# Kernel tuning notes

Measured on AMD Instinct MI355X. Metric: run time of the kernel, lower is better.

The kernel has to match this reference:

```python
import jax, jax.numpy as jnp
import numpy as np

MODEL_DIM = 1024
BATCH = 8
SEQ = 4096


def setup_inputs() -> dict:
    key = jax.random.key(0)
    x = jax.random.normal(key, (BATCH, SEQ, MODEL_DIM), dtype=jnp.float32)
    return {"input": x}


def _positional_encoding(seq_len: int, d_model: int, dtype) -> jnp.ndarray:
    # Faithful to the original: value = pos / 10000 ** (2*dim/d_model),
    # even dim -> sin(value), odd dim -> cos(value) (same raw-index frequency).
    pos = jnp.arange(seq_len, dtype=jnp.float32)[:, None]          # [S, 1]
    dim = jnp.arange(d_model, dtype=jnp.float32)[None, :]          # [1, D]
    inv_freq = jnp.power(jnp.float32(10000.0), -2.0 * dim / d_model)
    angle = pos * inv_freq                                          # [S, D]
    pe = jnp.where(jnp.arange(d_model)[None, :] % 2 == 0,
                   jnp.sin(angle), jnp.cos(angle))
    return pe.astype(dtype)


def reference(input) -> jnp.ndarray:
    B, S, D = input.shape
    pe = _positional_encoding(S, D, input.dtype)                    # [S, D]
    return input + pe[None, :, :]
```

## Files before the change

kernel.cpp:

```cpp
#include <hip/hip_runtime.h>
#include <stdint.h>


#define D_MODEL 1024
#define C_FREQ (-0.025952563241307517f)

__device__ float pe_val(int s, int d) {
    float angle = (float)s * exp2f(C_FREQ * (float)d);
    return (d & 1) ? cosf(angle) : sinf(angle);
}

__device__ uint32_t f2bf_rne(float f) {
    uint32_t b = __float_as_uint(f);
    return (b + 0x7FFFu + ((b >> 16) & 1u)) >> 16;
}

__global__ void detect_kernel(const uint16_t* in, int* flag) {
    __shared__ int bad;
    if (threadIdx.x == 0) bad = 0;
    __syncthreads();
    uint16_t u = in[threadIdx.x];
    int e = (u >> 7) & 0xFF;
    if (!(e == 0 || (e >= 96 && e <= 135))) bad = 1;
    __syncthreads();
    if (threadIdx.x == 0) *flag = (bad ? 0 : 1);
}

__global__ void pe_kernel(const void* vin, void* vout, const int* flag, int n) {
    __shared__ int bf16_s;
    if (threadIdx.x == 0) bf16_s = *flag;
    __syncthreads();
    const int is_bf16 = bf16_s;
    const int tid = blockIdx.x * blockDim.x + threadIdx.x;
    const int nth = gridDim.x * blockDim.x;

    if (is_bf16) {
        const uint32_t* in = (const uint32_t*)vin;
        uint32_t* out = (uint32_t*)vout;
        const int nw = n >> 1;
        for (int i = tid; i < nw; i += nth) {
            const int e0 = i << 1;
            const int d = e0 & (D_MODEL - 1);
            const int s = (e0 >> 10) & 4095;
            const float p0 = pe_val(s, d);
            const float p1 = pe_val(s, d + 1);
            const uint32_t w = in[i];
            const float x0 = __uint_as_float((w & 0xFFFFu) << 16);
            const float x1 = __uint_as_float(w & 0xFFFF0000u);
            out[i] = f2bf_rne(x0 + p0) | (f2bf_rne(x1 + p1) << 16);
        }
    } else {
        const float* in = (const float*)vin;
        float* out = (float*)vout;
        for (int i = tid; i < n; i += nth) {
            const int d = i & (D_MODEL - 1);
            const int s = (i >> 10) & 4095;
            out[i] = in[i] + pe_val(s, d);
        }
    }
}

extern "C" void kernel_launch(void* const* d_in, const int* in_sizes, int n_in,
                              void* d_out, int out_size, void* d_ws, size_t ws_size,
                              hipStream_t stream) {
    const void* x = d_in[0];
    int* flag = (int*)d_ws;
    detect_kernel<<<1, 256, 0, stream>>>((const uint16_t*)x, flag);
    pe_kernel<<<4096, 256, 0, stream>>>(x, d_out, flag, out_size);
}
```

Baseline: 235.9 us.

## Compute PE once per position and reuse across batch with vectorized nontemporal IO

Replaces the dtype-detecting grid-stride kernel with a single fp32 kernel in which each thread computes four PE values once and applies them to all eight batch rows. Loads and stores are 16-byte vectors with nontemporal hints, and the detect kernel launch is dropped. This removes redundant transcendental evaluation across the batch and the extra launch. In exchange it hardcodes the fp32 path and the fixed shapes.

After: 231.0 us. -2.1%, faster.

```diff
diff --git a/kernel.cpp b/kernel.cpp
--- a/kernel.cpp
+++ b/kernel.cpp
@@ -2,69 +2,47 @@
 #include <stdint.h>
 
 
-#define D_MODEL 1024
-#define C_FREQ (-0.025952563241307517f)
+constexpr int MODEL_DIM = 1024;
+constexpr int SEQ = 4096;
+constexpr int BATCH = 8;
+constexpr int SD = SEQ * MODEL_DIM;
+constexpr float C_FREQ = -0.025952563241307517f;
 
-__device__ float pe_val(int s, int d) {
-    float angle = (float)s * exp2f(C_FREQ * (float)d);
-    return (d & 1) ? cosf(angle) : sinf(angle);
-}
+typedef float v4f __attribute__((ext_vector_type(4)));
 
-__device__ uint32_t f2bf_rne(float f) {
-    uint32_t b = __float_as_uint(f);
-    return (b + 0x7FFFu + ((b >> 16) & 1u)) >> 16;
-}
+__global__ __launch_bounds__(256) void pe_add_kernel(
+    const float* __restrict__ xin, float* __restrict__ xout)
+{
+    const int t = blockIdx.x * blockDim.x + threadIdx.x;
+    const int s = t >> 8;
+    const int dbase = (t & 255) << 2;
 
-__global__ void detect_kernel(const uint16_t* in, int* flag) {
-    __shared__ int bad;
-    if (threadIdx.x == 0) bad = 0;
-    __syncthreads();
-    uint16_t u = in[threadIdx.x];
-    int e = (u >> 7) & 0xFF;
-    if (!(e == 0 || (e >= 96 && e <= 135))) bad = 1;
-    __syncthreads();
-    if (threadIdx.x == 0) *flag = (bad ? 0 : 1);
-}
+    const float pos = (float)s;
+    float pe[4];
+#pragma unroll
+    for (int j = 0; j < 4; ++j) {
+        const float angle = pos * exp2f(C_FREQ * (float)(dbase + j));
+        pe[j] = (j & 1) ? cosf(angle) : sinf(angle);
+    }
+    v4f pv;
+    pv.x = pe[0]; pv.y = pe[1]; pv.z = pe[2]; pv.w = pe[3];
 
-__global__ void pe_kernel(const void* vin, void* vout, const int* flag, int n) {
-    __shared__ int bf16_s;
-    if (threadIdx.x == 0) bf16_s = *flag;
-    __syncthreads();
-    const int is_bf16 = bf16_s;
-    const int tid = blockIdx.x * blockDim.x + threadIdx.x;
-    const int nth = gridDim.x * blockDim.x;
-
-    if (is_bf16) {
-        const uint32_t* in = (const uint32_t*)vin;
-        uint32_t* out = (uint32_t*)vout;
-        const int nw = n >> 1;
-        for (int i = tid; i < nw; i += nth) {
-            const int e0 = i << 1;
-            const int d = e0 & (D_MODEL - 1);
-            const int s = (e0 >> 10) & 4095;
-            const float p0 = pe_val(s, d);
-            const float p1 = pe_val(s, d + 1);
-            const uint32_t w = in[i];
-            const float x0 = __uint_as_float((w & 0xFFFFu) << 16);
-            const float x1 = __uint_as_float(w & 0xFFFF0000u);
-            out[i] = f2bf_rne(x0 + p0) | (f2bf_rne(x1 + p1) << 16);
-        }
-    } else {
-        const float* in = (const float*)vin;
-        float* out = (float*)vout;
-        for (int i = tid; i < n; i += nth) {
-            const int d = i & (D_MODEL - 1);
-            const int s = (i >> 10) & 4095;
-            out[i] = in[i] + pe_val(s, d);
-        }
+    const size_t base = (size_t)t * 4;
+#pragma unroll
+    for (int b = 0; b < BATCH; ++b) {
+        const size_t off = (size_t)b * (size_t)SD + base;
+        v4f x = __builtin_nontemporal_load((const v4f*)(xin + off));
+        x += pv;
+        __builtin_nontemporal_store(x, (v4f*)(xout + off));
     }
 }
 
 extern "C" void kernel_launch(void* const* d_in, const int* in_sizes, int n_in,
                               void* d_out, int out_size, void* d_ws, size_t ws_size,
                               hipStream_t stream) {
-    const void* x = d_in[0];
-    int* flag = (int*)d_ws;
-    detect_kernel<<<1, 256, 0, stream>>>((const uint16_t*)x, flag);
-    pe_kernel<<<4096, 256, 0, stream>>>(x, d_out, flag, out_size);
+    const float* x = (const float*)d_in[0];
+    float* out = (float*)d_out;
+    const int threads = 256;
+    const int blocks = (SD / 4) / threads;
+    pe_add_kernel<<<blocks, threads, 0, stream>>>(x, out);
 }
```
